# Kernel tuning notes

Measured on AMD Instinct MI355X. Metric: run time of the kernel, lower is better.

## Reference

```python
import jax, jax.numpy as jnp
import numpy as np

M, L, Q = 512, 256, 21


def setup_inputs() -> dict:
    key = jax.random.key(0)
    k1, k2, k3 = jax.random.split(key, 3)
    # one-hot encoded sequences (M, L, q)
    X_idx = jax.random.randint(k1, (M, L), 0, Q)
    X_oh = jax.nn.one_hot(X_idx, Q, dtype=jnp.float32)
    h_pos = 0.01 * jax.random.normal(k2, (L, Q), dtype=jnp.float32)
    J = 0.01 * jax.random.normal(k3, (L, L, Q, Q), dtype=jnp.float32)
    return {"X_oh": X_oh, "h_pos": h_pos, "J": J}


def reference(X_oh, h_pos, J):
    # z[m,i,a] = h[i,a] + sum_{j<i} sum_b J[i,j,b,a] * X[m,j,b]
    # (matches torch einsum 'mpq,pqr->mpr' over tril-gathered blocks)
    L_, q_ = h_pos.shape
    i_idx, j_idx = jnp.tril_indices(L_, k=-1)          # (P,), strictly lower, i sorted
    J_blocks = J[i_idx, j_idx]                          # (P, q, q)
    X_blocks = X_oh[:, j_idx]                           # (M, P, q)
    contrib = jnp.einsum('mpb,pba->mpa', X_blocks, J_blocks)  # (M, P, q)
    # scatter-add contributions to their target position i (sorted segments)
    agg = jax.ops.segment_sum(
        jnp.swapaxes(contrib, 0, 1),                    # (P, M, q)
        i_idx, num_segments=L_, indices_are_sorted=True
    )                                                   # (L, M, q)
    return h_pos[None, :, :] + jnp.swapaxes(agg, 0, 1)  # (M, L, q)
```

## Files before the change

kernel.cpp:

```cpp
#include <hip/hip_runtime.h>

#define L_DIM 256
#define M_DIM 512
#define Q_DIM 21
#define QQ    441
#define BLKB  1764
#define BUFS  2304
#define NBUF  8
#define DEPTH 6

#define GLD(src, dst, sz) __builtin_amdgcn_global_load_lds( \
    (const __attribute__((address_space(1))) void*)(src),   \
    (__attribute__((address_space(3))) void*)(dst), sz, 0, 0)

__global__ __launch_bounds__(64) void ardca_prep(const float* __restrict__ X_oh,
                                                 unsigned short* __restrict__ Xt) {
  int w = blockIdx.x;
  int lane = threadIdx.x;
  const float* base = X_oh + (size_t)w * (64 * Q_DIM);
  int rowbase = w * 64;
#pragma unroll 1
  for (int p = 0; p < 22; ++p) {
    int f = p * 63 + lane;
    float v = (lane < 63 && f < 1344) ? base[f] : 0.0f;
    unsigned long long mask = __ballot(v > 0.5f);
    if (lane < 3) {
      int rloc = 3 * p + lane;
      if (rloc < 64) {
        unsigned int bits = (unsigned int)((mask >> (21 * lane)) & 0x1FFFFFu);
        int x = bits ? __builtin_ctz(bits) : 0;
        int rr = rowbase + rloc;
        int m = rr >> 8, j = rr & 255;
        Xt[j * M_DIM + m] = (unsigned short)(x * 84);
      }
    }
  }
}

template <int USE_XT>
__global__ __launch_bounds__(64) void ardca_main(const float* __restrict__ Jm,
                                                 const float* __restrict__ h,
                                                 const unsigned short* __restrict__ Xt,
                                                 const float* __restrict__ X_oh,
                                                 float* __restrict__ out) {
  alignas(16) __shared__ char lds[NBUF * BUFS];
  int b = blockIdx.x;
  int c = b & 7;
  int r = b >> 3;
  int mg = r & 7;
  int i = ((31 - (r >> 3)) << 3) | c;
  int lane = threadIdx.x;
  int m = mg * 64 + lane;

  const char* Jrow = (const char*)Jm + (size_t)i * (256ull * BLKB);
  const char* XtB  = (const char*)Xt;

  float acc[Q_DIM];
#pragma unroll
  for (int a = 0; a < Q_DIM; ++a) acc[a] = 0.0f;

  auto STAGE = [&](int j) {
    char* buf = lds + (size_t)(j & 7) * BUFS;
    size_t bb = (size_t)(unsigned)j * BLKB;
    const char* src = Jrow + (bb & ~(size_t)15);
    GLD(src +        lane * 16, buf,        16);
    GLD(src + 1024 + lane * 16, buf + 1024, 16);
    if (USE_XT)
      GLD(XtB + (size_t)j * 1024 + mg * 128 + lane * 4, buf + 2048, 4);
  };

  auto CONSUME = [&](int j) {
    const char* buf = lds + (size_t)(j & 7) * BUFS;
    int off;
    if (USE_XT) {
      off = *(const unsigned short*)(buf + 2048 + 2 * lane);
    } else {
      const float* p = X_oh + ((size_t)m * L_DIM + j) * Q_DIM;
      int x = 0;
#pragma unroll
      for (int a = 0; a < Q_DIM; ++a) x = (p[a] > 0.5f) ? a : x;
      off = x * 84;
    }
    const float* row = (const float*)(buf + ((j & 3) << 2) + off);
#pragma unroll
    for (int k = 0; k < 10; ++k) {
      acc[2 * k]     += row[2 * k];
      acc[2 * k + 1] += row[2 * k + 1];
    }
    acc[20] += row[20];
  };

  int P = (i < DEPTH) ? i : DEPTH;
  for (int j = 0; j < P; ++j) STAGE(j);
  int jt = i - DEPTH; if (jt < 0) jt = 0;

#pragma unroll 1
  for (int j = 0; j < jt; ++j) {
    STAGE(j + DEPTH);
    if (USE_XT) {
      asm volatile("s_waitcnt vmcnt(18)" ::: "memory");
    } else {
      asm volatile("s_waitcnt vmcnt(0)" ::: "memory");
    }
    __builtin_amdgcn_sched_barrier(0);
    CONSUME(j);
  }
  asm volatile("s_waitcnt vmcnt(0)" ::: "memory");
  __builtin_amdgcn_sched_barrier(0);
#pragma unroll 1
  for (int j = jt; j < i; ++j) CONSUME(j);

  const float* hp = h + i * Q_DIM;
  float* o = out + ((size_t)m * L_DIM + i) * Q_DIM;
#pragma unroll
  for (int a = 0; a < Q_DIM; ++a) o[a] = acc[a] + hp[a];
}

extern "C" void kernel_launch(void* const* d_in, const int* in_sizes, int n_in,
                              void* d_out, int out_size, void* d_ws, size_t ws_size,
                              hipStream_t stream) {
  const float* X_oh = (const float*)d_in[0];
  const float* h    = (const float*)d_in[1];
  const float* Jm   = (const float*)d_in[2];
  float* out        = (float*)d_out;
  unsigned short* Xt = (unsigned short*)d_ws;

  if (ws_size >= (size_t)M_DIM * L_DIM * sizeof(unsigned short)) {
    ardca_prep<<<2048, 64, 0, stream>>>(X_oh, Xt);
    ardca_main<1><<<2048, 64, 0, stream>>>(Jm, h, Xt, X_oh, out);
  } else {
    ardca_main<0><<<2048, 64, 0, stream>>>(Jm, h, Xt, X_oh, out);
  }
}
```

Baseline: 218.9 us.

## Split output columns across half-waves and double grid with shallower pipeline

```diff
diff --git a/kernel.cpp b/kernel.cpp
--- a/kernel.cpp
+++ b/kernel.cpp
@@ -3,11 +3,11 @@
 #define L_DIM 256
 #define M_DIM 512
 #define Q_DIM 21
-#define QQ    441
-#define BLKB  1764
-#define BUFS  2304
-#define NBUF  8
-#define DEPTH 6
+#define BLKB   1764
+#define SLOT   1920
+#define IDXOFF 1792
+#define NBUF   4
+#define DEPTH  3
 
 #define GLD(src, dst, sz) __builtin_amdgcn_global_load_lds( \
     (const __attribute__((address_space(1))) void*)(src),   \
@@ -19,7 +19,7 @@
   int lane = threadIdx.x;
   const float* base = X_oh + (size_t)w * (64 * Q_DIM);
   int rowbase = w * 64;
-#pragma unroll 1
+#pragma unroll 4
   for (int p = 0; p < 22; ++p) {
     int f = p * 63 + lane;
     float v = (lane < 63 && f < 1344) ? base[f] : 0.0f;
@@ -43,37 +43,41 @@
                                                  const unsigned short* __restrict__ Xt,
                                                  const float* __restrict__ X_oh,
                                                  float* __restrict__ out) {
-  alignas(16) __shared__ char lds[NBUF * BUFS];
+  alignas(16) __shared__ char lds[NBUF * SLOT];
   int b = blockIdx.x;
   int c = b & 7;
   int r = b >> 3;
-  int mg = r & 7;
-  int i = ((31 - (r >> 3)) << 3) | c;
+  int mg = r & 15;
+  int i = ((31 - (r >> 4)) << 3) | c;
   int lane = threadIdx.x;
-  int m = mg * 64 + lane;
+  int ml = lane & 31;
+  int ah = lane >> 5;
+  int m = mg * 32 + ml;
 
   const char* Jrow = (const char*)Jm + (size_t)i * (256ull * BLKB);
   const char* XtB  = (const char*)Xt;
 
-  float acc[Q_DIM];
+  float acc[12];
+  const float* hp = h + i * Q_DIM + ah * 12;
 #pragma unroll
-  for (int a = 0; a < Q_DIM; ++a) acc[a] = 0.0f;
+  for (int k = 0; k < 12; ++k) acc[k] = (ah == 0 || k < 9) ? hp[k] : 0.0f;
 
   auto STAGE = [&](int j) {
-    char* buf = lds + (size_t)(j & 7) * BUFS;
-    size_t bb = (size_t)(unsigned)j * BLKB;
-    const char* src = Jrow + (bb & ~(size_t)15);
-    GLD(src +        lane * 16, buf,        16);
-    GLD(src + 1024 + lane * 16, buf + 1024, 16);
-    if (USE_XT)
-      GLD(XtB + (size_t)j * 1024 + mg * 128 + lane * 4, buf + 2048, 4);
+    char* buf = lds + (j & (NBUF - 1)) * SLOT;
+    unsigned bb = (unsigned)j * BLKB;
+    const char* src = Jrow + (bb & ~15u);
+    GLD(src + lane * 16, buf, 16);
+    if (lane < 48) GLD(src + 1024 + lane * 16, buf + 1024, 16);
+    if (USE_XT) {
+      if (lane < 16) GLD(XtB + j * 1024 + mg * 64 + lane * 4, buf + IDXOFF, 4);
+    }
   };
 
   auto CONSUME = [&](int j) {
-    const char* buf = lds + (size_t)(j & 7) * BUFS;
+    const char* buf = lds + (j & (NBUF - 1)) * SLOT;
     int off;
     if (USE_XT) {
-      off = *(const unsigned short*)(buf + 2048 + 2 * lane);
+      off = *(const unsigned short*)(buf + IDXOFF + 2 * ml);
     } else {
       const float* p = X_oh + ((size_t)m * L_DIM + j) * Q_DIM;
       int x = 0;
@@ -81,13 +85,9 @@
       for (int a = 0; a < Q_DIM; ++a) x = (p[a] > 0.5f) ? a : x;
       off = x * 84;
     }
-    const float* row = (const float*)(buf + ((j & 3) << 2) + off);
+    const float* row = (const float*)(buf + ((j & 3) << 2) + off) + ah * 12;
 #pragma unroll
-    for (int k = 0; k < 10; ++k) {
-      acc[2 * k]     += row[2 * k];
-      acc[2 * k + 1] += row[2 * k + 1];
-    }
-    acc[20] += row[20];
+    for (int k = 0; k < 12; ++k) acc[k] += row[k];
   };
 
   int P = (i < DEPTH) ? i : DEPTH;
@@ -98,7 +98,7 @@
   for (int j = 0; j < jt; ++j) {
     STAGE(j + DEPTH);
     if (USE_XT) {
-      asm volatile("s_waitcnt vmcnt(18)" ::: "memory");
+      asm volatile("s_waitcnt vmcnt(9)" ::: "memory");
     } else {
       asm volatile("s_waitcnt vmcnt(0)" ::: "memory");
     }
@@ -110,10 +110,14 @@
 #pragma unroll 1
   for (int j = jt; j < i; ++j) CONSUME(j);
 
-  const float* hp = h + i * Q_DIM;
-  float* o = out + ((size_t)m * L_DIM + i) * Q_DIM;
+  float* o = out + ((size_t)m * L_DIM + i) * Q_DIM + ah * 12;
+  if (ah == 0) {
 #pragma unroll
-  for (int a = 0; a < Q_DIM; ++a) o[a] = acc[a] + hp[a];
+    for (int k = 0; k < 12; ++k) o[k] = acc[k];
+  } else {
+#pragma unroll
+    for (int k = 0; k < 9; ++k) o[k] = acc[k];
+  }
 }
 
 extern "C" void kernel_launch(void* const* d_in, const int* in_sizes, int n_in,
@@ -127,8 +131,8 @@
 
   if (ws_size >= (size_t)M_DIM * L_DIM * sizeof(unsigned short)) {
     ardca_prep<<<2048, 64, 0, stream>>>(X_oh, Xt);
-    ardca_main<1><<<2048, 64, 0, stream>>>(Jm, h, Xt, X_oh, out);
+    ardca_main<1><<<4096, 64, 0, stream>>>(Jm, h, Xt, X_oh, out);
   } else {
-    ardca_main<0><<<2048, 64, 0, stream>>>(Jm, h, Xt, X_oh, out);
+    ardca_main<0><<<4096, 64, 0, stream>>>(Jm, h, Xt, X_oh, out);
   }
 }
```

Result: slower. 236.5 us (+8.1%).
